# Optimization experiments

Hardware: AMD Instinct MI355X
Metric: run time of the kernel (lower is better)

Reference implementation:

```python
import jax, jax.numpy as jnp
import numpy as np

K = 6
N_SAMPLES = 5
NOISE_FACTOR = 1.0
TEMP = 1.0
N_ITERS = 5
EPS = 1e-20
B = 131072
D_LAT = 16
D_FEAT = 8


def _sinkhorn(log_alpha):
    # iterative row/column logsumexp normalization on [M, K, K]
    for _ in range(N_ITERS):
        log_alpha = log_alpha - jax.scipy.special.logsumexp(log_alpha, axis=2, keepdims=True)
        log_alpha = log_alpha - jax.scipy.special.logsumexp(log_alpha, axis=1, keepdims=True)
    return jnp.exp(log_alpha)


def setup_inputs() -> dict:
    key = jax.random.key(0)
    ks = jax.random.split(key, 5)
    latent = jax.random.normal(ks[0], (B, D_LAT), dtype=jnp.float32)
    seq = jax.random.normal(ks[1], (B, K, D_FEAT), dtype=jnp.float32)
    noise_u = jax.random.uniform(ks[2], (N_SAMPLES * B, K, K), dtype=jnp.float32)
    W_sink = jax.random.normal(ks[3], (D_LAT, K * K), dtype=jnp.float32) * 0.1
    b_sink = jnp.zeros((K * K,), dtype=jnp.float32)
    W_mask = jax.random.normal(ks[4], (D_LAT, K), dtype=jnp.float32) * 0.1
    b_mask = jnp.zeros((K,), dtype=jnp.float32)
    return {"latent": latent, "seq": seq, "noise_u": noise_u,
            "W_sink": W_sink, "b_sink": b_sink, "W_mask": W_mask, "b_mask": b_mask}


def reference(latent, seq, noise_u, W_sink, b_sink, W_mask, b_mask):
    b = latent.shape[0]
    # sinknet: Linear(latent_dim, K*K) -> [B, K, K]
    log_alpha = (latent @ W_sink + b_sink).reshape(b, K, K)
    # gumbel_sinkhorn: tile over samples (sample-major, like torch .repeat)
    la = jnp.tile(log_alpha, (N_SAMPLES, 1, 1))  # [S*B, K, K]
    gumbel = -jnp.log(EPS - jnp.log(noise_u + EPS))
    la = (la + gumbel * NOISE_FACTOR) / TEMP
    sink = _sinkhorn(la)  # [S*B, K, K]
    # inv_soft_pers_flattened == transpose of each KxK matrix (same flat order)
    P = jnp.swapaxes(sink, 1, 2)
    seq_tiled = jnp.tile(seq, (N_SAMPLES, 1, 1))  # [S*B, K, D]
    ordered = jnp.matmul(P, seq_tiled)  # [S*B, K, D]
    # masknet: Linear + Softmax(dim=1)
    stopping = jax.nn.softmax(latent @ W_mask + b_mask, axis=1)  # [B, K]
    return ordered, stopping
```

## Files before the change

### kernel.cpp

```cpp
#include <hip/hip_runtime.h>

namespace {

constexpr int K     = 6;
constexpr int KK    = 36;
constexpr int DF    = 8;
constexpr int DLAT  = 16;
constexpr int NS    = 5;
constexpr int B     = 131072;
constexpr int M     = NS * B;
constexpr float EPS = 1e-20f;

__global__ __launch_bounds__(256) void sink_kernel(
    const float* __restrict__ latent,
    const float* __restrict__ seq,
    const float* __restrict__ noise,
    const float* __restrict__ W_sink,
    const float* __restrict__ b_sink,
    float* __restrict__ out)
{
    const int m = blockIdx.x * 256 + threadIdx.x;
    const int b = (int)((unsigned)m / 5u);
    const int s = m - b * 5;
    const size_t row = (size_t)s * B + b;

    float lat[DLAT];
    const float4* lat4 = reinterpret_cast<const float4*>(latent + (size_t)b * DLAT);
    #pragma unroll
    for (int k = 0; k < 4; ++k) {
        float4 v = lat4[k];
        lat[k*4+0] = v.x; lat[k*4+1] = v.y; lat[k*4+2] = v.z; lat[k*4+3] = v.w;
    }

    float la[KK];
    #pragma unroll
    for (int i = 0; i < KK; ++i) la[i] = b_sink[i];
    #pragma unroll
    for (int k = 0; k < DLAT; ++k) {
        const float lv = lat[k];
        #pragma unroll
        for (int i = 0; i < KK; ++i)
            la[i] = fmaf(lv, W_sink[k*KK + i], la[i]);
    }

    float p[KK];
    {
        const float4* n4 = reinterpret_cast<const float4*>(noise + row * KK);
        float u[KK];
        #pragma unroll
        for (int q = 0; q < 9; ++q) {
            float4 v = n4[q];
            u[q*4+0] = v.x; u[q*4+1] = v.y; u[q*4+2] = v.z; u[q*4+3] = v.w;
        }
        #pragma unroll
        for (int i = 0; i < KK; ++i)
            p[i] = __expf(la[i] - __logf(EPS - __logf(u[i] + EPS)));
    }

    #pragma unroll
    for (int it = 0; it < 5; ++it) {
        #pragma unroll
        for (int i = 0; i < K; ++i) {
            const float sum = ((p[i*K+0] + p[i*K+1]) + (p[i*K+2] + p[i*K+3]))
                            + (p[i*K+4] + p[i*K+5]);
            const float r = __builtin_amdgcn_rcpf(sum);
            #pragma unroll
            for (int j = 0; j < K; ++j) p[i*K+j] *= r;
        }
        #pragma unroll
        for (int j = 0; j < K; ++j) {
            const float sum = ((p[0*K+j] + p[1*K+j]) + (p[2*K+j] + p[3*K+j]))
                            + (p[4*K+j] + p[5*K+j]);
            const float r = __builtin_amdgcn_rcpf(sum);
            #pragma unroll
            for (int i = 0; i < K; ++i) p[i*K+j] *= r;
        }
    }

    float o[K*DF];
    #pragma unroll
    for (int i = 0; i < K*DF; ++i) o[i] = 0.f;

    const float4* s4 = reinterpret_cast<const float4*>(seq + (size_t)b * (K*DF));
    #pragma unroll
    for (int j = 0; j < K; ++j) {
        float4 a0 = s4[j*2 + 0];
        float4 a1 = s4[j*2 + 1];
        float srow[DF] = {a0.x, a0.y, a0.z, a0.w, a1.x, a1.y, a1.z, a1.w};
        #pragma unroll
        for (int i = 0; i < K; ++i) {
            const float pv = p[j*K + i];
            #pragma unroll
            for (int d = 0; d < DF; ++d)
                o[i*DF + d] = fmaf(pv, srow[d], o[i*DF + d]);
        }
    }

    float4* o4 = reinterpret_cast<float4*>(out + row * (K*DF));
    #pragma unroll
    for (int q = 0; q < 12; ++q) {
        float4 v;
        v.x = o[q*4+0]; v.y = o[q*4+1]; v.z = o[q*4+2]; v.w = o[q*4+3];
        o4[q] = v;
    }
}

__global__ __launch_bounds__(256) void mask_kernel(
    const float* __restrict__ latent,
    const float* __restrict__ W_mask,
    const float* __restrict__ b_mask,
    float* __restrict__ outp)
{
    const int b = blockIdx.x * 256 + threadIdx.x;
    if (b >= B) return;

    float lat[DLAT];
    const float4* lat4 = reinterpret_cast<const float4*>(latent + (size_t)b * DLAT);
    #pragma unroll
    for (int k = 0; k < 4; ++k) {
        float4 v = lat4[k];
        lat[k*4+0] = v.x; lat[k*4+1] = v.y; lat[k*4+2] = v.z; lat[k*4+3] = v.w;
    }

    float v[K];
    #pragma unroll
    for (int i = 0; i < K; ++i) v[i] = b_mask[i];
    #pragma unroll
    for (int k = 0; k < DLAT; ++k) {
        const float lv = lat[k];
        #pragma unroll
        for (int i = 0; i < K; ++i)
            v[i] = fmaf(lv, W_mask[k*K + i], v[i]);
    }

    float mx = v[0];
    #pragma unroll
    for (int i = 1; i < K; ++i) mx = fmaxf(mx, v[i]);
    float sum = 0.f;
    #pragma unroll
    for (int i = 0; i < K; ++i) { v[i] = __expf(v[i] - mx); sum += v[i]; }
    const float inv = 1.f / sum;
    #pragma unroll
    for (int i = 0; i < K; ++i) v[i] *= inv;

    float2* o2 = reinterpret_cast<float2*>(outp + (size_t)b * K);
    o2[0] = make_float2(v[0], v[1]);
    o2[1] = make_float2(v[2], v[3]);
    o2[2] = make_float2(v[4], v[5]);
}

}

extern "C" void kernel_launch(void* const* d_in, const int* in_sizes, int n_in,
                              void* d_out, int out_size, void* d_ws, size_t ws_size,
                              hipStream_t stream) {
    const float* latent = (const float*)d_in[0];
    const float* seq    = (const float*)d_in[1];
    const float* noise  = (const float*)d_in[2];
    const float* W_sink = (const float*)d_in[3];
    const float* b_sink = (const float*)d_in[4];
    const float* W_mask = (const float*)d_in[5];
    const float* b_mask = (const float*)d_in[6];
    float* out = (float*)d_out;

    sink_kernel<<<M / 256, 256, 0, stream>>>(latent, seq, noise, W_sink, b_sink, out);
    mask_kernel<<<B / 256, 256, 0, stream>>>(latent, W_mask, b_mask,
                                             out + (size_t)M * K * DF);
}
```

Before: 76.80 us.

## Precompute exp of sinkhorn logits per batch and fold gumbel into reciprocal

```diff
diff --git a/kernel.cpp b/kernel.cpp
--- a/kernel.cpp
+++ b/kernel.cpp
@@ -11,7 +11,143 @@
 constexpr int M     = NS * B;
 constexpr float EPS = 1e-20f;
 
+__global__ __launch_bounds__(256) void prep_kernel(
+    const float* __restrict__ latent,
+    const float* __restrict__ W_sink,
+    const float* __restrict__ b_sink,
+    const float* __restrict__ W_mask,
+    const float* __restrict__ b_mask,
+    float* __restrict__ ela,
+    float* __restrict__ stopping)
+{
+    const int b = blockIdx.x * 256 + threadIdx.x;
+
+    float lat[DLAT];
+    const float4* lat4 = reinterpret_cast<const float4*>(latent + (size_t)b * DLAT);
+    #pragma unroll
+    for (int k = 0; k < 4; ++k) {
+        float4 v = lat4[k];
+        lat[k*4+0] = v.x; lat[k*4+1] = v.y; lat[k*4+2] = v.z; lat[k*4+3] = v.w;
+    }
+
+    float la[KK];
+    #pragma unroll
+    for (int i = 0; i < KK; ++i) la[i] = b_sink[i];
+    #pragma unroll
+    for (int k = 0; k < DLAT; ++k) {
+        const float lv = lat[k];
+        #pragma unroll
+        for (int i = 0; i < KK; ++i)
+            la[i] = fmaf(lv, W_sink[k*KK + i], la[i]);
+    }
+
+    float4* e4 = reinterpret_cast<float4*>(ela + (size_t)b * KK);
+    #pragma unroll
+    for (int q = 0; q < 9; ++q) {
+        float4 v;
+        v.x = __expf(la[q*4+0]); v.y = __expf(la[q*4+1]);
+        v.z = __expf(la[q*4+2]); v.w = __expf(la[q*4+3]);
+        e4[q] = v;
+    }
+
+    float v[K];
+    #pragma unroll
+    for (int i = 0; i < K; ++i) v[i] = b_mask[i];
+    #pragma unroll
+    for (int k = 0; k < DLAT; ++k) {
+        const float lv = lat[k];
+        #pragma unroll
+        for (int i = 0; i < K; ++i)
+            v[i] = fmaf(lv, W_mask[k*K + i], v[i]);
+    }
+    float mx = v[0];
+    #pragma unroll
+    for (int i = 1; i < K; ++i) mx = fmaxf(mx, v[i]);
+    float sum = 0.f;
+    #pragma unroll
+    for (int i = 0; i < K; ++i) { v[i] = __expf(v[i] - mx); sum += v[i]; }
+    const float inv = __builtin_amdgcn_rcpf(sum);
+    float2* o2 = reinterpret_cast<float2*>(stopping + (size_t)b * K);
+    o2[0] = make_float2(v[0]*inv, v[1]*inv);
+    o2[1] = make_float2(v[2]*inv, v[3]*inv);
+    o2[2] = make_float2(v[4]*inv, v[5]*inv);
+}
+
 __global__ __launch_bounds__(256) void sink_kernel(
+    const float* __restrict__ seq,
+    const float* __restrict__ noise,
+    const float* __restrict__ ela,
+    float* __restrict__ out)
+{
+    const int m = blockIdx.x * 256 + threadIdx.x;
+    const int b = (int)((unsigned)m / 5u);
+    const int s = m - b * 5;
+    const size_t row = (size_t)s * B + b;
+
+    float p[KK];
+    {
+        const float4* e4 = reinterpret_cast<const float4*>(ela + (size_t)b * KK);
+        const float4* n4 = reinterpret_cast<const float4*>(noise + row * KK);
+        #pragma unroll
+        for (int q = 0; q < 9; ++q) {
+            float4 e = e4[q];
+            float4 u = n4[q];
+            p[q*4+0] = e.x * __builtin_amdgcn_rcpf(EPS - __logf(u.x + EPS));
+            p[q*4+1] = e.y * __builtin_amdgcn_rcpf(EPS - __logf(u.y + EPS));
+            p[q*4+2] = e.z * __builtin_amdgcn_rcpf(EPS - __logf(u.z + EPS));
+            p[q*4+3] = e.w * __builtin_amdgcn_rcpf(EPS - __logf(u.w + EPS));
+        }
+    }
+
+    #pragma unroll
+    for (int it = 0; it < 5; ++it) {
+        #pragma unroll
+        for (int i = 0; i < K; ++i) {
+            const float sum = ((p[i*K+0] + p[i*K+1]) + (p[i*K+2] + p[i*K+3]))
+                            + (p[i*K+4] + p[i*K+5]);
+            const float r = __builtin_amdgcn_rcpf(sum);
+            #pragma unroll
+            for (int j = 0; j < K; ++j) p[i*K+j] *= r;
+        }
+        #pragma unroll
+        for (int j = 0; j < K; ++j) {
+            const float sum = ((p[0*K+j] + p[1*K+j]) + (p[2*K+j] + p[3*K+j]))
+                            + (p[4*K+j] + p[5*K+j]);
+            const float r = __builtin_amdgcn_rcpf(sum);
+            #pragma unroll
+            for (int i = 0; i < K; ++i) p[i*K+j] *= r;
+        }
+    }
+
+    float o[K*DF];
+    #pragma unroll
+    for (int i = 0; i < K*DF; ++i) o[i] = 0.f;
+
+    const float4* s4 = reinterpret_cast<const float4*>(seq + (size_t)b * (K*DF));
+    #pragma unroll
+    for (int j = 0; j < K; ++j) {
+        float4 a0 = s4[j*2 + 0];
+        float4 a1 = s4[j*2 + 1];
+        float srow[DF] = {a0.x, a0.y, a0.z, a0.w, a1.x, a1.y, a1.z, a1.w};
+        #pragma unroll
+        for (int i = 0; i < K; ++i) {
+            const float pv = p[j*K + i];
+            #pragma unroll
+            for (int d = 0; d < DF; ++d)
+                o[i*DF + d] = fmaf(pv, srow[d], o[i*DF + d]);
+        }
+    }
+
+    float4* o4 = reinterpret_cast<float4*>(out + row * (K*DF));
+    #pragma unroll
+    for (int q = 0; q < 12; ++q) {
+        float4 v;
+        v.x = o[q*4+0]; v.y = o[q*4+1]; v.z = o[q*4+2]; v.w = o[q*4+3];
+        o4[q] = v;
+    }
+}
+
+__global__ __launch_bounds__(256) void sink_mono_kernel(
     const float* __restrict__ latent,
     const float* __restrict__ seq,
     const float* __restrict__ noise,
@@ -46,15 +182,14 @@
     float p[KK];
     {
         const float4* n4 = reinterpret_cast<const float4*>(noise + row * KK);
-        float u[KK];
         #pragma unroll
         for (int q = 0; q < 9; ++q) {
-            float4 v = n4[q];
-            u[q*4+0] = v.x; u[q*4+1] = v.y; u[q*4+2] = v.z; u[q*4+3] = v.w;
-        }
-        #pragma unroll
-        for (int i = 0; i < KK; ++i)
-            p[i] = __expf(la[i] - __logf(EPS - __logf(u[i] + EPS)));
+            float4 u = n4[q];
+            p[q*4+0] = __expf(la[q*4+0]) * __builtin_amdgcn_rcpf(EPS - __logf(u.x + EPS));
+            p[q*4+1] = __expf(la[q*4+1]) * __builtin_amdgcn_rcpf(EPS - __logf(u.y + EPS));
+            p[q*4+2] = __expf(la[q*4+2]) * __builtin_amdgcn_rcpf(EPS - __logf(u.z + EPS));
+            p[q*4+3] = __expf(la[q*4+3]) * __builtin_amdgcn_rcpf(EPS - __logf(u.w + EPS));
+        }
     }
 
     #pragma unroll
@@ -80,7 +215,6 @@
     float o[K*DF];
     #pragma unroll
     for (int i = 0; i < K*DF; ++i) o[i] = 0.f;
-
     const float4* s4 = reinterpret_cast<const float4*>(seq + (size_t)b * (K*DF));
     #pragma unroll
     for (int j = 0; j < K; ++j) {
@@ -95,7 +229,6 @@
                 o[i*DF + d] = fmaf(pv, srow[d], o[i*DF + d]);
         }
     }
-
     float4* o4 = reinterpret_cast<float4*>(out + row * (K*DF));
     #pragma unroll
     for (int q = 0; q < 12; ++q) {
@@ -121,7 +254,6 @@
         float4 v = lat4[k];
         lat[k*4+0] = v.x; lat[k*4+1] = v.y; lat[k*4+2] = v.z; lat[k*4+3] = v.w;
     }
-
     float v[K];
     #pragma unroll
     for (int i = 0; i < K; ++i) v[i] = b_mask[i];
@@ -132,7 +264,6 @@
         for (int i = 0; i < K; ++i)
             v[i] = fmaf(lv, W_mask[k*K + i], v[i]);
     }
-
     float mx = v[0];
     #pragma unroll
     for (int i = 1; i < K; ++i) mx = fmaxf(mx, v[i]);
@@ -140,13 +271,10 @@
     #pragma unroll
     for (int i = 0; i < K; ++i) { v[i] = __expf(v[i] - mx); sum += v[i]; }
     const float inv = 1.f / sum;
-    #pragma unroll
-    for (int i = 0; i < K; ++i) v[i] *= inv;
-
     float2* o2 = reinterpret_cast<float2*>(outp + (size_t)b * K);
-    o2[0] = make_float2(v[0], v[1]);
-    o2[1] = make_float2(v[2], v[3]);
-    o2[2] = make_float2(v[4], v[5]);
+    o2[0] = make_float2(v[0]*inv, v[1]*inv);
+    o2[1] = make_float2(v[2]*inv, v[3]*inv);
+    o2[2] = make_float2(v[4]*inv, v[5]*inv);
 }
 
 }
@@ -161,9 +289,18 @@
     const float* b_sink = (const float*)d_in[4];
     const float* W_mask = (const float*)d_in[5];
     const float* b_mask = (const float*)d_in[6];
-    float* out = (float*)d_out;
-
-    sink_kernel<<<M / 256, 256, 0, stream>>>(latent, seq, noise, W_sink, b_sink, out);
-    mask_kernel<<<B / 256, 256, 0, stream>>>(latent, W_mask, b_mask,
-                                             out + (size_t)M * K * DF);
-}
+    float* out      = (float*)d_out;
+    float* stopping = out + (size_t)M * K * DF;
+
+    const size_t need = (size_t)B * KK * sizeof(float);
+    if (ws_size >= need) {
+        float* ela = (float*)d_ws;
+        prep_kernel<<<B / 256, 256, 0, stream>>>(latent, W_sink, b_sink,
+                                                 W_mask, b_mask, ela, stopping);
+        sink_kernel<<<M / 256, 256, 0, stream>>>(seq, noise, ela, out);
+    } else {
+        sink_mono_kernel<<<M / 256, 256, 0, stream>>>(latent, seq, noise,
+                                                      W_sink, b_sink, out);
+        mask_kernel<<<B / 256, 256, 0, stream>>>(latent, W_mask, b_mask, stopping);
+    }
+}
```

Result: slower. 101.0 us (+31.6%).

## Fuse mask softmax into sink kernel and loop samples per batch row

Applied to the files above, without the earlier changes.

```diff
diff --git a/kernel.cpp b/kernel.cpp
--- a/kernel.cpp
+++ b/kernel.cpp
@@ -11,18 +11,18 @@
 constexpr int M     = NS * B;
 constexpr float EPS = 1e-20f;
 
-__global__ __launch_bounds__(256) void sink_kernel(
+__global__ __launch_bounds__(256) void fused_kernel(
     const float* __restrict__ latent,
     const float* __restrict__ seq,
     const float* __restrict__ noise,
     const float* __restrict__ W_sink,
     const float* __restrict__ b_sink,
-    float* __restrict__ out)
+    const float* __restrict__ W_mask,
+    const float* __restrict__ b_mask,
+    float* __restrict__ out,
+    float* __restrict__ stopping)
 {
-    const int m = blockIdx.x * 256 + threadIdx.x;
-    const int b = (int)((unsigned)m / 5u);
-    const int s = m - b * 5;
-    const size_t row = (size_t)s * B + b;
+    const int b = blockIdx.x * 256 + threadIdx.x;
 
     float lat[DLAT];
     const float4* lat4 = reinterpret_cast<const float4*>(latent + (size_t)b * DLAT);
@@ -32,121 +32,109 @@
         lat[k*4+0] = v.x; lat[k*4+1] = v.y; lat[k*4+2] = v.z; lat[k*4+3] = v.w;
     }
 
-    float la[KK];
+    float ela[KK];
     #pragma unroll
-    for (int i = 0; i < KK; ++i) la[i] = b_sink[i];
+    for (int i = 0; i < KK; ++i) ela[i] = b_sink[i];
     #pragma unroll
     for (int k = 0; k < DLAT; ++k) {
         const float lv = lat[k];
         #pragma unroll
         for (int i = 0; i < KK; ++i)
-            la[i] = fmaf(lv, W_sink[k*KK + i], la[i]);
+            ela[i] = fmaf(lv, W_sink[k*KK + i], ela[i]);
     }
 
-    float p[KK];
     {
-        const float4* n4 = reinterpret_cast<const float4*>(noise + row * KK);
-        float u[KK];
+        float v[K];
         #pragma unroll
-        for (int q = 0; q < 9; ++q) {
-            float4 v = n4[q];
-            u[q*4+0] = v.x; u[q*4+1] = v.y; u[q*4+2] = v.z; u[q*4+3] = v.w;
+        for (int i = 0; i < K; ++i) v[i] = b_mask[i];
+        #pragma unroll
+        for (int k = 0; k < DLAT; ++k) {
+            const float lv = lat[k];
+            #pragma unroll
+            for (int i = 0; i < K; ++i)
+                v[i] = fmaf(lv, W_mask[k*K + i], v[i]);
         }
+        float mx = v[0];
         #pragma unroll
-        for (int i = 0; i < KK; ++i)
-            p[i] = __expf(la[i] - __logf(EPS - __logf(u[i] + EPS)));
+        for (int i = 1; i < K; ++i) mx = fmaxf(mx, v[i]);
+        float sum = 0.f;
+        #pragma unroll
+        for (int i = 0; i < K; ++i) { v[i] = __expf(v[i] - mx); sum += v[i]; }
+        const float inv = __builtin_amdgcn_rcpf(sum);
+        float2* o2 = reinterpret_cast<float2*>(stopping + (size_t)b * K);
+        o2[0] = make_float2(v[0]*inv, v[1]*inv);
+        o2[1] = make_float2(v[2]*inv, v[3]*inv);
+        o2[2] = make_float2(v[4]*inv, v[5]*inv);
     }
 
     #pragma unroll
-    for (int it = 0; it < 5; ++it) {
+    for (int i = 0; i < KK; ++i) ela[i] = __expf(ela[i]);
+
+    float sq[K*DF];
+    const float4* s4 = reinterpret_cast<const float4*>(seq + (size_t)b * (K*DF));
+    #pragma unroll
+    for (int q = 0; q < 12; ++q) {
+        float4 v = s4[q];
+        sq[q*4+0] = v.x; sq[q*4+1] = v.y; sq[q*4+2] = v.z; sq[q*4+3] = v.w;
+    }
+
+    #pragma unroll
+    for (int s = 0; s < NS; ++s) {
+        const size_t row = (size_t)s * B + b;
+
+        float p[KK];
+        {
+            const float4* n4 = reinterpret_cast<const float4*>(noise + row * KK);
+            #pragma unroll
+            for (int q = 0; q < 9; ++q) {
+                float4 u = n4[q];
+                p[q*4+0] = ela[q*4+0] * __builtin_amdgcn_rcpf(EPS - __logf(u.x + EPS));
+                p[q*4+1] = ela[q*4+1] * __builtin_amdgcn_rcpf(EPS - __logf(u.y + EPS));
+                p[q*4+2] = ela[q*4+2] * __builtin_amdgcn_rcpf(EPS - __logf(u.z + EPS));
+                p[q*4+3] = ela[q*4+3] * __builtin_amdgcn_rcpf(EPS - __logf(u.w + EPS));
+            }
+        }
+
+        #pragma unroll
+        for (int it = 0; it < 5; ++it) {
+            #pragma unroll
+            for (int i = 0; i < K; ++i) {
+                const float sum = ((p[i*K+0] + p[i*K+1]) + (p[i*K+2] + p[i*K+3]))
+                                + (p[i*K+4] + p[i*K+5]);
+                const float r = __builtin_amdgcn_rcpf(sum);
+                #pragma unroll
+                for (int j = 0; j < K; ++j) p[i*K+j] *= r;
+            }
+            #pragma unroll
+            for (int j = 0; j < K; ++j) {
+                const float sum = ((p[0*K+j] + p[1*K+j]) + (p[2*K+j] + p[3*K+j]))
+                                + (p[4*K+j] + p[5*K+j]);
+                const float r = __builtin_amdgcn_rcpf(sum);
+                #pragma unroll
+                for (int i = 0; i < K; ++i) p[i*K+j] *= r;
+            }
+        }
+
+        float4* o4 = reinterpret_cast<float4*>(out + row * (K*DF));
         #pragma unroll
         for (int i = 0; i < K; ++i) {
-            const float sum = ((p[i*K+0] + p[i*K+1]) + (p[i*K+2] + p[i*K+3]))
-                            + (p[i*K+4] + p[i*K+5]);
-            const float r = __builtin_amdgcn_rcpf(sum);
+            float orow[DF];
             #pragma unroll
-            for (int j = 0; j < K; ++j) p[i*K+j] *= r;
-        }
-        #pragma unroll
-        for (int j = 0; j < K; ++j) {
-            const float sum = ((p[0*K+j] + p[1*K+j]) + (p[2*K+j] + p[3*K+j]))
-                            + (p[4*K+j] + p[5*K+j]);
-            const float r = __builtin_amdgcn_rcpf(sum);
+            for (int d = 0; d < DF; ++d) orow[d] = 0.f;
             #pragma unroll
-            for (int i = 0; i < K; ++i) p[i*K+j] *= r;
+            for (int j = 0; j < K; ++j) {
+                const float pv = p[j*K + i];
+                #pragma unroll
+                for (int d = 0; d < DF; ++d)
+                    orow[d] = fmaf(pv, sq[j*DF + d], orow[d]);
+            }
+            float4 v0, v1;
+            v0.x = orow[0]; v0.y = orow[1]; v0.z = orow[2]; v0.w = orow[3];
+            v1.x = orow[4]; v1.y = orow[5]; v1.z = orow[6]; v1.w = orow[7];
+            o4[i*2 + 0] = v0;
+            o4[i*2 + 1] = v1;
         }
     }
-
-    float o[K*DF];
-    #pragma unroll
-    for (int i = 0; i < K*DF; ++i) o[i] = 0.f;
-
-    const float4* s4 = reinterpret_cast<const float4*>(seq + (size_t)b * (K*DF));
-    #pragma unroll
-    for (int j = 0; j < K; ++j) {
-        float4 a0 = s4[j*2 + 0];
-        float4 a1 = s4[j*2 + 1];
-        float srow[DF] = {a0.x, a0.y, a0.z, a0.w, a1.x, a1.y, a1.z, a1.w};
-        #pragma unroll
-        for (int i = 0; i < K; ++i) {
-            const float pv = p[j*K + i];
-            #pragma unroll
-            for (int d = 0; d < DF; ++d)
-                o[i*DF + d] = fmaf(pv, srow[d], o[i*DF + d]);
-        }
-    }
-
-    float4* o4 = reinterpret_cast<float4*>(out + row * (K*DF));
-    #pragma unroll
-    for (int q = 0; q < 12; ++q) {
-        float4 v;
-        v.x = o[q*4+0]; v.y = o[q*4+1]; v.z = o[q*4+2]; v.w = o[q*4+3];
-        o4[q] = v;
-    }
-}
-
-__global__ __launch_bounds__(256) void mask_kernel(
-    const float* __restrict__ latent,
-    const float* __restrict__ W_mask,
-    const float* __restrict__ b_mask,
-    float* __restrict__ outp)
-{
-    const int b = blockIdx.x * 256 + threadIdx.x;
-    if (b >= B) return;
-
-    float lat[DLAT];
-    const float4* lat4 = reinterpret_cast<const float4*>(latent + (size_t)b * DLAT);
-    #pragma unroll
-    for (int k = 0; k < 4; ++k) {
-        float4 v = lat4[k];
-        lat[k*4+0] = v.x; lat[k*4+1] = v.y; lat[k*4+2] = v.z; lat[k*4+3] = v.w;
-    }
-
-    float v[K];
-    #pragma unroll
-    for (int i = 0; i < K; ++i) v[i] = b_mask[i];
-    #pragma unroll
-    for (int k = 0; k < DLAT; ++k) {
-        const float lv = lat[k];
-        #pragma unroll
-        for (int i = 0; i < K; ++i)
-            v[i] = fmaf(lv, W_mask[k*K + i], v[i]);
-    }
-
-    float mx = v[0];
-    #pragma unroll
-    for (int i = 1; i < K; ++i) mx = fmaxf(mx, v[i]);
-    float sum = 0.f;
-    #pragma unroll
-    for (int i = 0; i < K; ++i) { v[i] = __expf(v[i] - mx); sum += v[i]; }
-    const float inv = 1.f / sum;
-    #pragma unroll
-    for (int i = 0; i < K; ++i) v[i] *= inv;
-
-    float2* o2 = reinterpret_cast<float2*>(outp + (size_t)b * K);
-    o2[0] = make_float2(v[0], v[1]);
-    o2[1] = make_float2(v[2], v[3]);
-    o2[2] = make_float2(v[4], v[5]);
 }
 
 }
@@ -161,9 +149,10 @@
     const float* b_sink = (const float*)d_in[4];
     const float* W_mask = (const float*)d_in[5];
     const float* b_mask = (const float*)d_in[6];
-    float* out = (float*)d_out;
+    float* out      = (float*)d_out;
+    float* stopping = out + (size_t)M * K * DF;
 
-    sink_kernel<<<M / 256, 256, 0, stream>>>(latent, seq, noise, W_sink, b_sink, out);
-    mask_kernel<<<B / 256, 256, 0, stream>>>(latent, W_mask, b_mask,
-                                             out + (size_t)M * K * DF);
+    fused_kernel<<<B / 256, 256, 0, stream>>>(latent, seq, noise,
+                                              W_sink, b_sink, W_mask, b_mask,
+                                              out, stopping);
 }
```

Result: slower. 94.55 us (+23.1%).
